# Performance work log

Hardware: AMD Instinct MI355X
Metric: run time of the kernel (lower is better)

Reference implementation:

```python
import jax, jax.numpy as jnp
import numpy as np

N_LAGS = 64
UNBIASED = False


def setup_inputs() -> dict:
    key = jax.random.key(0)
    X = jax.random.normal(key, (4096, 8192), dtype=jnp.float32)
    return {"X": X}


def reference(X) -> jnp.ndarray:
    # X: [B, T]
    B, T = X.shape
    Xc = X - jnp.mean(X, axis=1, keepdims=True)  # center per sequence
    acs = []
    for k in range(N_LAGS + 1):  # small fixed loop over lags
        denom = (T - k) if UNBIASED else T
        # sum_{t} Xc[b, t] * Xc[b, t+k]
        ac_k = jnp.einsum('bt,bt->b', Xc[:, : T - k], Xc[:, k:]) / denom
        acs.append(ac_k)
    Xautocorr = jnp.stack(acs, axis=1)  # [B, n_lags+1]
    # normalize lags 1..n_lags by lag-0 variance
    return Xautocorr[:, 1:] / Xautocorr[:, :1]
```

## Files before the change

kernel.cpp:

```cpp
#include <hip/hip_runtime.h>


typedef __bf16 bf16x8 __attribute__((ext_vector_type(8)));
typedef float f32x16 __attribute__((ext_vector_type(16)));
typedef unsigned int uint32;

#define T_LEN 8192
#define WPB 4
#define GB_STRIDE 34
#define GB_SHORTS (96 * GB_STRIDE)

__device__ __forceinline__ uint32 cvtpk(float lo, float hi) {
  uint32 r;
  asm("v_cvt_pk_bf16_f32 %0, %1, %2" : "=v"(r) : "v"(lo), "v"(hi));
  return r;
}
__device__ __forceinline__ short f2bf(float f) {
  uint32 u = __builtin_bit_cast(uint32, f);
  return (short)((u + 0x7fffu + ((u >> 16) & 1u)) >> 16);
}
__device__ __forceinline__ float bf2f(short h) {
  uint32 u = ((uint32)(unsigned short)h) << 16;
  return __builtin_bit_cast(float, u);
}

__global__ __launch_bounds__(WPB * 64, 4)
void autocorr_kernel(const float* __restrict__ X, float* __restrict__ out, int nrows) {
  __shared__ short gb_all[WPB * GB_SHORTS];
  const int wave = threadIdx.x >> 6;
  const int lane = threadIdx.x & 63;
  const int row = blockIdx.x * WPB + wave;
  if (row >= nrows) return;
  short* gb = gb_all + wave * GB_SHORTS;

  const int m = lane & 31;
  const int sh = lane >> 5;
  const float* __restrict__ base = X + (size_t)row * T_LEN + (sh << 8) + m;

  f32x16 g0 = {}, g1 = {}, g2 = {};
  float ssum = 0.f;

  float e0 = base[0],   e1 = base[32],  e2 = base[64],  e3 = base[96];
  float e4 = base[128], e5 = base[160], e6 = base[192], e7 = base[224];
  uint32 u0 = cvtpk(e0, e1);

#pragma unroll 4
  for (int c = 0; c < 16; ++c) {
    float n0 = 0.f, n1 = 0.f, n2 = 0.f, n3 = 0.f;
    float n4 = 0.f, n5 = 0.f, n6 = 0.f, n7 = 0.f;
    if (c < 15) {
      const float* pn = base + ((c + 1) << 9);
      n0 = pn[0];   n1 = pn[32];  n2 = pn[64];  n3 = pn[96];
      n4 = pn[128]; n5 = pn[160]; n6 = pn[192]; n7 = pn[224];
    }

    ssum += ((e0 + e1) + (e2 + e3)) + ((e4 + e5) + (e6 + e7));
    uint32 u1 = cvtpk(e2, e3), u2 = cvtpk(e4, e5), u3 = cvtpk(e6, e7);
    uint32 u0n = cvtpk(n0, n1);
    uint32 u4 = (uint32)__shfl_xor((int)(sh ? u0 : u0n), 32, 64);

    int4 a4 = make_int4((int)u0, (int)u1, (int)u2, (int)u3);
    int4 b1;
    b1.x = (int)((u0 >> 16) | (u1 << 16));
    b1.y = (int)((u1 >> 16) | (u2 << 16));
    b1.z = (int)((u2 >> 16) | (u3 << 16));
    b1.w = (int)((u3 >> 16) | (u4 << 16));
    int4 b2 = make_int4((int)u1, (int)u2, (int)u3, (int)u4);
    bf16x8 fa = __builtin_bit_cast(bf16x8, a4);
    bf16x8 f1 = __builtin_bit_cast(bf16x8, b1);
    bf16x8 f2 = __builtin_bit_cast(bf16x8, b2);
    g0 = __builtin_amdgcn_mfma_f32_32x32x16_bf16(fa, fa, g0, 0, 0, 0);
    g1 = __builtin_amdgcn_mfma_f32_32x32x16_bf16(fa, f1, g1, 0, 0, 0);
    g2 = __builtin_amdgcn_mfma_f32_32x32x16_bf16(fa, f2, g2, 0, 0, 0);

    e0 = n0; e1 = n1; e2 = n2; e3 = n3; e4 = n4; e5 = n5; e6 = n6; e7 = n7;
    u0 = u0n;
  }

  for (int d = 32; d > 0; d >>= 1) ssum += __shfl_xor(ssum, d, 64);

#pragma unroll
  for (int v = 0; v < 16; ++v) {
    int rm = (v & 3) + (sh << 2) + ((v >> 2) << 3);
    gb[(rm)      * GB_STRIDE + m] = f2bf(g0[v]);
    gb[(32 + rm) * GB_STRIDE + m] = f2bf(g1[v]);
    gb[(64 + rm) * GB_STRIDE + m] = f2bf(g2[v]);
  }

  int k = lane + 1;
  int s2 = k & 31, q = k >> 5;
  float ck = 0.f;
#pragma unroll 4
  for (int mm = 0; mm < 32; ++mm) {
    int ms = mm + s2;
    int dd = q + (ms >> 5);
    ck += bf2f(gb[(dd * 32 + mm) * GB_STRIDE + (ms & 31)]);
  }
  float c0 = 0.f;
#pragma unroll 4
  for (int mm = 0; mm < 32; ++mm) c0 += bf2f(gb[mm * GB_STRIDE + mm]);

  float P = X[(size_t)row * T_LEN + lane];
  float Q = X[(size_t)row * T_LEN + (T_LEN - 1 - lane)];
  for (int d = 1; d < 64; d <<= 1) {
    float tp = __shfl_up(P, (unsigned)d, 64);
    float tq = __shfl_up(Q, (unsigned)d, 64);
    if (lane >= d) { P += tp; Q += tq; }
  }
  float mu = ssum * (1.0f / (float)T_LEN);
  float Ck = ck - mu * (2.f * ssum - P - Q) + (float)(T_LEN - k) * mu * mu;
  float C0 = c0 - mu * 2.f * ssum + (float)T_LEN * mu * mu;
  out[(size_t)row * 64 + lane] = Ck / C0;
}

extern "C" void kernel_launch(void* const* d_in, const int* in_sizes, int n_in,
                              void* d_out, int out_size, void* d_ws, size_t ws_size,
                              hipStream_t stream) {
  const float* X = (const float*)d_in[0];
  float* out = (float*)d_out;
  int nrows = in_sizes[0] / T_LEN;
  dim3 grid((nrows + WPB - 1) / WPB);
  autocorr_kernel<<<grid, dim3(WPB * 64), 0, stream>>>(X, out, nrows);
}
```

Before: 189.3 us.

## Split each row across two waves using 16x16x32 MFMA with five lag blocks

Each row is now handled by two waves, each covering half the sequence, and the block reduces their partial Gram blocks and sums through shared memory after a barrier. The 32x32x16 MFMA with three lag blocks is replaced by 16x16x32 MFMA with five shifted operand blocks. Each wave loads 12 values per chunk, including overlapping halo values, instead of prefetching and shuffling across lane halves. The intent is more memory parallelism, with twice the waves in flight and occupancy raised to 8. The cost is redundant halo loads, a __syncthreads, and half the waves sitting idle during the final reduction.

```diff
diff --git a/kernel.cpp b/kernel.cpp
--- a/kernel.cpp
+++ b/kernel.cpp
@@ -2,13 +2,12 @@
 
 
 typedef __bf16 bf16x8 __attribute__((ext_vector_type(8)));
-typedef float f32x16 __attribute__((ext_vector_type(16)));
+typedef float f32x4 __attribute__((ext_vector_type(4)));
 typedef unsigned int uint32;
 
 #define T_LEN 8192
-#define WPB 4
-#define GB_STRIDE 34
-#define GB_SHORTS (96 * GB_STRIDE)
+#define GST 18
+#define GB_SHORTS (80 * GST)
 
 __device__ __forceinline__ uint32 cvtpk(float lo, float hi) {
   uint32 r;
@@ -24,93 +23,115 @@
   return __builtin_bit_cast(float, u);
 }
 
-__global__ __launch_bounds__(WPB * 64, 4)
+__global__ __launch_bounds__(256, 8)
 void autocorr_kernel(const float* __restrict__ X, float* __restrict__ out, int nrows) {
-  __shared__ short gb_all[WPB * GB_SHORTS];
-  const int wave = threadIdx.x >> 6;
+  __shared__ short gb_all[4 * GB_SHORTS];
+  __shared__ float ss[4];
+  const int wv = threadIdx.x >> 6;
   const int lane = threadIdx.x & 63;
-  const int row = blockIdx.x * WPB + wave;
-  if (row >= nrows) return;
-  short* gb = gb_all + wave * GB_SHORTS;
+  const int pr = wv >> 1;
+  const int h  = wv & 1;
+  const int row = blockIdx.x * 2 + pr;
+  const int rowc = row < nrows ? row : 0;
 
-  const int m = lane & 31;
-  const int sh = lane >> 5;
-  const float* __restrict__ base = X + (size_t)row * T_LEN + (sh << 8) + m;
+  short* gme = gb_all + wv * GB_SHORTS;
 
-  f32x16 g0 = {}, g1 = {}, g2 = {};
+  const int m  = lane & 15;
+  const int lg = lane >> 4;
+  const float* __restrict__ base =
+      X + (size_t)rowc * T_LEN + (h << 12) + (lg << 7) + m;
+
+  f32x4 g0 = {}, g1 = {}, g2 = {}, g3 = {}, g4 = {};
   float ssum = 0.f;
 
-  float e0 = base[0],   e1 = base[32],  e2 = base[64],  e3 = base[96];
-  float e4 = base[128], e5 = base[160], e6 = base[192], e7 = base[224];
-  uint32 u0 = cvtpk(e0, e1);
+#define BODY()                                                                 \
+  {                                                                            \
+    ssum += ((e0 + e1) + (e2 + e3)) + ((e4 + e5) + (e6 + e7));                 \
+    uint32 u0 = cvtpk(e0, e1), u1 = cvtpk(e2, e3), u2 = cvtpk(e4, e5);         \
+    uint32 u3 = cvtpk(e6, e7), u4 = cvtpk(e8, e9), u5 = cvtpk(e10, e11);       \
+    uint32 a01 = (u0 >> 16) | (u1 << 16), a12 = (u1 >> 16) | (u2 << 16);       \
+    uint32 a23 = (u2 >> 16) | (u3 << 16), a34 = (u3 >> 16) | (u4 << 16);       \
+    uint32 a45 = (u4 >> 16) | (u5 << 16);                                      \
+    int4 A4 = make_int4((int)u0, (int)u1, (int)u2, (int)u3);                   \
+    int4 C1 = make_int4((int)a01, (int)a12, (int)a23, (int)a34);               \
+    int4 C2 = make_int4((int)u1, (int)u2, (int)u3, (int)u4);                   \
+    int4 C3 = make_int4((int)a12, (int)a23, (int)a34, (int)a45);               \
+    int4 C4 = make_int4((int)u2, (int)u3, (int)u4, (int)u5);                   \
+    bf16x8 fa = __builtin_bit_cast(bf16x8, A4);                                \
+    bf16x8 f1 = __builtin_bit_cast(bf16x8, C1);                                \
+    bf16x8 f2 = __builtin_bit_cast(bf16x8, C2);                                \
+    bf16x8 f3 = __builtin_bit_cast(bf16x8, C3);                                \
+    bf16x8 f4 = __builtin_bit_cast(bf16x8, C4);                                \
+    g0 = __builtin_amdgcn_mfma_f32_16x16x32_bf16(fa, fa, g0, 0, 0, 0);         \
+    g1 = __builtin_amdgcn_mfma_f32_16x16x32_bf16(fa, f1, g1, 0, 0, 0);         \
+    g2 = __builtin_amdgcn_mfma_f32_16x16x32_bf16(fa, f2, g2, 0, 0, 0);         \
+    g3 = __builtin_amdgcn_mfma_f32_16x16x32_bf16(fa, f3, g3, 0, 0, 0);         \
+    g4 = __builtin_amdgcn_mfma_f32_16x16x32_bf16(fa, f4, g4, 0, 0, 0);         \
+  }
 
-#pragma unroll 4
-  for (int c = 0; c < 16; ++c) {
-    float n0 = 0.f, n1 = 0.f, n2 = 0.f, n3 = 0.f;
-    float n4 = 0.f, n5 = 0.f, n6 = 0.f, n7 = 0.f;
-    if (c < 15) {
-      const float* pn = base + ((c + 1) << 9);
-      n0 = pn[0];   n1 = pn[32];  n2 = pn[64];  n3 = pn[96];
-      n4 = pn[128]; n5 = pn[160]; n6 = pn[192]; n7 = pn[224];
-    }
-
-    ssum += ((e0 + e1) + (e2 + e3)) + ((e4 + e5) + (e6 + e7));
-    uint32 u1 = cvtpk(e2, e3), u2 = cvtpk(e4, e5), u3 = cvtpk(e6, e7);
-    uint32 u0n = cvtpk(n0, n1);
-    uint32 u4 = (uint32)__shfl_xor((int)(sh ? u0 : u0n), 32, 64);
-
-    int4 a4 = make_int4((int)u0, (int)u1, (int)u2, (int)u3);
-    int4 b1;
-    b1.x = (int)((u0 >> 16) | (u1 << 16));
-    b1.y = (int)((u1 >> 16) | (u2 << 16));
-    b1.z = (int)((u2 >> 16) | (u3 << 16));
-    b1.w = (int)((u3 >> 16) | (u4 << 16));
-    int4 b2 = make_int4((int)u1, (int)u2, (int)u3, (int)u4);
-    bf16x8 fa = __builtin_bit_cast(bf16x8, a4);
-    bf16x8 f1 = __builtin_bit_cast(bf16x8, b1);
-    bf16x8 f2 = __builtin_bit_cast(bf16x8, b2);
-    g0 = __builtin_amdgcn_mfma_f32_32x32x16_bf16(fa, fa, g0, 0, 0, 0);
-    g1 = __builtin_amdgcn_mfma_f32_32x32x16_bf16(fa, f1, g1, 0, 0, 0);
-    g2 = __builtin_amdgcn_mfma_f32_32x32x16_bf16(fa, f2, g2, 0, 0, 0);
-
-    e0 = n0; e1 = n1; e2 = n2; e3 = n3; e4 = n4; e5 = n5; e6 = n6; e7 = n7;
-    u0 = u0n;
+#pragma unroll 1
+  for (int c = 0; c < 7; ++c) {
+    const float* p = base + (c << 9);
+    float e0 = p[0],   e1 = p[16],  e2 = p[32],   e3 = p[48];
+    float e4 = p[64],  e5 = p[80],  e6 = p[96],   e7 = p[112];
+    float e8 = p[128], e9 = p[144], e10 = p[160], e11 = p[176];
+    BODY()
   }
+  {
+    const float* p = base + (7 << 9);
+    float e0 = p[0],  e1 = p[16], e2 = p[32],  e3 = p[48];
+    float e4 = p[64], e5 = p[80], e6 = p[96],  e7 = p[112];
+    float e8 = 0.f, e9 = 0.f, e10 = 0.f, e11 = 0.f;
+    if (!(h && lg == 3)) { e8 = p[128]; e9 = p[144]; e10 = p[160]; e11 = p[176]; }
+    BODY()
+  }
+#undef BODY
 
   for (int d = 32; d > 0; d >>= 1) ssum += __shfl_xor(ssum, d, 64);
 
 #pragma unroll
-  for (int v = 0; v < 16; ++v) {
-    int rm = (v & 3) + (sh << 2) + ((v >> 2) << 3);
-    gb[(rm)      * GB_STRIDE + m] = f2bf(g0[v]);
-    gb[(32 + rm) * GB_STRIDE + m] = f2bf(g1[v]);
-    gb[(64 + rm) * GB_STRIDE + m] = f2bf(g2[v]);
+  for (int v = 0; v < 4; ++v) {
+    int rm = (lg << 2) + v;
+    gme[(rm)      * GST + m] = f2bf(g0[v]);
+    gme[(16 + rm) * GST + m] = f2bf(g1[v]);
+    gme[(32 + rm) * GST + m] = f2bf(g2[v]);
+    gme[(48 + rm) * GST + m] = f2bf(g3[v]);
+    gme[(64 + rm) * GST + m] = f2bf(g4[v]);
   }
+  if (lane == 0) ss[wv] = ssum;
+  __syncthreads();
 
-  int k = lane + 1;
-  int s2 = k & 31, q = k >> 5;
-  float ck = 0.f;
+  if (h == 0 && row < nrows) {
+    const short* ga = gb_all + (pr * 2) * GB_SHORTS;
+    const short* gh = ga + GB_SHORTS;
+    float S = ss[pr * 2] + ss[pr * 2 + 1];
+
+    int k = lane + 1;
+    int s2 = k & 15, q = k >> 4;
+    float ck = 0.f;
 #pragma unroll 4
-  for (int mm = 0; mm < 32; ++mm) {
-    int ms = mm + s2;
-    int dd = q + (ms >> 5);
-    ck += bf2f(gb[(dd * 32 + mm) * GB_STRIDE + (ms & 31)]);
+    for (int mm = 0; mm < 16; ++mm) {
+      int ms = mm + s2;
+      int idx = ((q + (ms >> 4)) * 16 + mm) * GST + (ms & 15);
+      ck += bf2f(ga[idx]) + bf2f(gh[idx]);
+    }
+    float c0 = 0.f;
+#pragma unroll 4
+    for (int mm = 0; mm < 16; ++mm)
+      c0 += bf2f(ga[mm * GST + mm]) + bf2f(gh[mm * GST + mm]);
+
+    float P = X[(size_t)row * T_LEN + lane];
+    float Q = X[(size_t)row * T_LEN + (T_LEN - 1 - lane)];
+    for (int d = 1; d < 64; d <<= 1) {
+      float tp = __shfl_up(P, (unsigned)d, 64);
+      float tq = __shfl_up(Q, (unsigned)d, 64);
+      if (lane >= d) { P += tp; Q += tq; }
+    }
+    float mu = S * (1.0f / (float)T_LEN);
+    float Ck = ck - mu * (2.f * S - P - Q) + (float)(T_LEN - k) * mu * mu;
+    float C0 = c0 - mu * 2.f * S + (float)T_LEN * mu * mu;
+    out[(size_t)row * 64 + lane] = Ck / C0;
   }
-  float c0 = 0.f;
-#pragma unroll 4
-  for (int mm = 0; mm < 32; ++mm) c0 += bf2f(gb[mm * GB_STRIDE + mm]);
-
-  float P = X[(size_t)row * T_LEN + lane];
-  float Q = X[(size_t)row * T_LEN + (T_LEN - 1 - lane)];
-  for (int d = 1; d < 64; d <<= 1) {
-    float tp = __shfl_up(P, (unsigned)d, 64);
-    float tq = __shfl_up(Q, (unsigned)d, 64);
-    if (lane >= d) { P += tp; Q += tq; }
-  }
-  float mu = ssum * (1.0f / (float)T_LEN);
-  float Ck = ck - mu * (2.f * ssum - P - Q) + (float)(T_LEN - k) * mu * mu;
-  float C0 = c0 - mu * 2.f * ssum + (float)T_LEN * mu * mu;
-  out[(size_t)row * 64 + lane] = Ck / C0;
 }
 
 extern "C" void kernel_launch(void* const* d_in, const int* in_sizes, int n_in,
@@ -119,6 +140,6 @@
   const float* X = (const float*)d_in[0];
   float* out = (float*)d_out;
   int nrows = in_sizes[0] / T_LEN;
-  dim3 grid((nrows + WPB - 1) / WPB);
-  autocorr_kernel<<<grid, dim3(WPB * 64), 0, stream>>>(X, out, nrows);
+  dim3 grid((nrows + 1) / 2);
+  autocorr_kernel<<<grid, dim3(256), 0, stream>>>(X, out, nrows);
 }
```

Result: no change. 190.2 us (+0.4%).

## Stage row chunks into LDS via async global_load_lds double buffering

Applied to the files above, without the earlier changes.

Replaces direct per-lane strided global loads with async global-to-LDS copies of 512-float chunks, double-buffered per wave with explicit vmcnt waits. Each lane loads the tail elements it needs for the lag window directly, which removes the cross-half shuffle. The intent is coalesced 16-byte loads with deeper prefetch that overlap the MFMA work. The risks are added LDS traffic and bank conflicts on the strided reads, plus a fragile waitcnt accounting that mixes these copies with ordinary global loads.

```diff
diff --git a/kernel.cpp b/kernel.cpp
--- a/kernel.cpp
+++ b/kernel.cpp
@@ -9,6 +9,7 @@
 #define WPB 4
 #define GB_STRIDE 34
 #define GB_SHORTS (96 * GB_STRIDE)
+#define WAVE_SMEM 6528
 
 __device__ __forceinline__ uint32 cvtpk(float lo, float hi) {
   uint32 r;
@@ -24,41 +25,55 @@
   return __builtin_bit_cast(float, u);
 }
 
+__device__ __forceinline__ void stage1k(const float* src, float* ldsdst) {
+  __builtin_amdgcn_global_load_lds(
+      (const __attribute__((address_space(1))) void*)src,
+      (__attribute__((address_space(3))) void*)ldsdst, 16, 0, 0);
+}
+
 __global__ __launch_bounds__(WPB * 64, 4)
 void autocorr_kernel(const float* __restrict__ X, float* __restrict__ out, int nrows) {
-  __shared__ short gb_all[WPB * GB_SHORTS];
+  __shared__ __align__(16) char smem[WPB * WAVE_SMEM];
   const int wave = threadIdx.x >> 6;
   const int lane = threadIdx.x & 63;
   const int row = blockIdx.x * WPB + wave;
   if (row >= nrows) return;
-  short* gb = gb_all + wave * GB_SHORTS;
+  float* buf = (float*)(smem + wave * WAVE_SMEM);
+  short* gb  = (short*)(smem + wave * WAVE_SMEM);
 
   const int m = lane & 31;
   const int sh = lane >> 5;
-  const float* __restrict__ base = X + (size_t)row * T_LEN + (sh << 8) + m;
+  const float* __restrict__ rb = X + (size_t)row * T_LEN;
+  const float* __restrict__ ep = rb + (sh << 8) + m + 256;
 
   f32x16 g0 = {}, g1 = {}, g2 = {};
   float ssum = 0.f;
 
-  float e0 = base[0],   e1 = base[32],  e2 = base[64],  e3 = base[96];
-  float e4 = base[128], e5 = base[160], e6 = base[192], e7 = base[224];
-  uint32 u0 = cvtpk(e0, e1);
+  stage1k(rb + 4 * lane,        buf);
+  stage1k(rb + 256 + 4 * lane,  buf + 256);
+  float x8 = ep[0], x9 = ep[32];
+  stage1k(rb + 512 + 4 * lane,  buf + 512);
+  stage1k(rb + 768 + 4 * lane,  buf + 768);
 
-#pragma unroll 4
+#pragma unroll
   for (int c = 0; c < 16; ++c) {
-    float n0 = 0.f, n1 = 0.f, n2 = 0.f, n3 = 0.f;
-    float n4 = 0.f, n5 = 0.f, n6 = 0.f, n7 = 0.f;
-    if (c < 15) {
-      const float* pn = base + ((c + 1) << 9);
-      n0 = pn[0];   n1 = pn[32];  n2 = pn[64];  n3 = pn[96];
-      n4 = pn[128]; n5 = pn[160]; n6 = pn[192]; n7 = pn[224];
+    if (c == 15) asm volatile("s_waitcnt vmcnt(0)" ::: "memory");
+    else         asm volatile("s_waitcnt vmcnt(2)" ::: "memory");
+
+    const float* lb = buf + (c & 1) * 512 + (sh << 8) + m;
+    float e0 = lb[0],   e1 = lb[32],  e2 = lb[64],  e3 = lb[96];
+    float e4 = lb[128], e5 = lb[160], e6 = lb[192], e7 = lb[224];
+
+    float nx8 = 0.f, nx9 = 0.f;
+    if (c + 1 < 15) { nx8 = ep[(c + 1) << 9]; nx9 = ep[((c + 1) << 9) + 32]; }
+    else if (c + 1 == 15) {
+      if (!sh) { nx8 = ep[15 << 9]; nx9 = ep[(15 << 9) + 32]; }
     }
 
     ssum += ((e0 + e1) + (e2 + e3)) + ((e4 + e5) + (e6 + e7));
-    uint32 u1 = cvtpk(e2, e3), u2 = cvtpk(e4, e5), u3 = cvtpk(e6, e7);
-    uint32 u0n = cvtpk(n0, n1);
-    uint32 u4 = (uint32)__shfl_xor((int)(sh ? u0 : u0n), 32, 64);
-
+    uint32 u0 = cvtpk(e0, e1), u1 = cvtpk(e2, e3);
+    uint32 u2 = cvtpk(e4, e5), u3 = cvtpk(e6, e7);
+    uint32 u4 = cvtpk(x8, x9);
     int4 a4 = make_int4((int)u0, (int)u1, (int)u2, (int)u3);
     int4 b1;
     b1.x = (int)((u0 >> 16) | (u1 << 16));
@@ -73,8 +88,14 @@
     g1 = __builtin_amdgcn_mfma_f32_32x32x16_bf16(fa, f1, g1, 0, 0, 0);
     g2 = __builtin_amdgcn_mfma_f32_32x32x16_bf16(fa, f2, g2, 0, 0, 0);
 
-    e0 = n0; e1 = n1; e2 = n2; e3 = n3; e4 = n4; e5 = n5; e6 = n6; e7 = n7;
-    u0 = u0n;
+    if (c + 2 <= 15) {
+      __builtin_amdgcn_sched_barrier(0);
+      const float* s = rb + ((c + 2) << 9);
+      float* d = buf + (c & 1) * 512;
+      stage1k(s + 4 * lane,       d);
+      stage1k(s + 256 + 4 * lane, d + 256);
+    }
+    x8 = nx8; x9 = nx9;
   }
 
   for (int d = 32; d > 0; d >>= 1) ssum += __shfl_xor(ssum, d, 64);
```

After: 224.0 us. 18.3% more time.
